# Kernel optimization log

Hardware: AMD Instinct MI355X
Metric: run time of the kernel (lower is better)

Reference implementation:

```python
import jax, jax.numpy as jnp
import numpy as np

H = 256        # hidden_channels
G = 13         # num_input_geofeature
E = 100000     # number of 2nd-order triplets
N = 50000      # num_nodes
DEPTH = 3      # finaldepth
EPS = 1e-5     # BatchNorm eps


def setup_inputs() -> dict:
    key = jax.random.key(0)
    ks = jax.random.split(key, 10)
    d_in = 3 * H + G  # 781
    return {
        "node_feature": jax.random.normal(ks[0], (N, H), jnp.float32),
        "geo_encoding": jax.random.normal(ks[1], (E, G), jnp.float32),
        "edge_index_2rd": jax.random.randint(ks[2], (3, E), 0, N),
        "edx_ij": jax.random.randint(ks[3], (E,), 0, 2 * E),
        "edx_jk": jax.random.randint(ks[4], (E,), 0, 2 * E),
        "att": jax.random.uniform(ks[5], (4,), jnp.float32),
        # 4 branches: layer0 (d_in->H) + DEPTH layers (H->H), xavier-ish init, zero bias
        "W0": jax.random.normal(ks[6], (4, d_in, H), jnp.float32) * (1.0 / np.sqrt(d_in)),
        "b0": jnp.zeros((4, H), jnp.float32),
        "Wh": jax.random.normal(ks[7], (4, DEPTH, H, H), jnp.float32) * (1.0 / np.sqrt(H)),
        "bh": jnp.zeros((4, DEPTH, H), jnp.float32),
        # BatchNorm (eval mode): affine params + running stats, one per layer per branch
        "gamma": jnp.ones((4, DEPTH + 1, H), jnp.float32),
        "beta": jnp.zeros((4, DEPTH + 1, H), jnp.float32),
        "run_mean": jnp.zeros((4, DEPTH + 1, H), jnp.float32),
        "run_var": jnp.ones((4, DEPTH + 1, H), jnp.float32),
        "num_edge_inside": E,
        "num_nodes": N,
    }


def _bn(h, g, b, m, v):
    return (h - m) * jax.lax.rsqrt(v + EPS) * g + b


def reference(node_feature, geo_encoding, edge_index_2rd, edx_ij, edx_jk, att,
              W0, b0, Wh, bh, gamma, beta, run_mean, run_var,
              num_edge_inside, num_nodes):
    i, j, k = edge_index_2rd[0], edge_index_2rd[1], edge_index_2rd[2]
    # gather node triplets + geo features -> [E, 3H+G]
    x = jnp.concatenate(
        [node_feature[i], node_feature[j], node_feature[k], geo_encoding], axis=-1)

    m_ij = edx_ij < num_edge_inside
    m_jk = edx_jk < num_edge_inside
    # 4 mutually-exclusive, exhaustive routing masks: [4, E]
    masks = jnp.stack([m_ij & m_jk, m_ij & ~m_jk, ~m_ij & m_jk, ~m_ij & ~m_jk])

    x_output = jnp.zeros((x.shape[0], H), x.dtype)
    for br in range(4):  # fixed small branch count
        h = jax.nn.relu(_bn(x @ W0[br] + b0[br],
                            gamma[br, 0], beta[br, 0], run_mean[br, 0], run_var[br, 0]))
        for l in range(DEPTH):
            h = jax.nn.relu(_bn(h @ Wh[br, l] + bh[br, l],
                                gamma[br, l + 1], beta[br, l + 1],
                                run_mean[br, l + 1], run_var[br, l + 1]))
        h = jax.nn.leaky_relu(h) * att[br]
        x_output = x_output + jnp.where(masks[br][:, None], h, jnp.zeros((), h.dtype))
    # scatter_add over target node index i -> [num_nodes, H]
    return jax.ops.segment_sum(x_output, i, num_segments=num_nodes)
```

## Files before the change

kernel.cpp:

```cpp
#include <hip/hip_runtime.h>
#include <hip/hip_bf16.h>
#include <stdint.h>

#define HCH 256
#define GEO 13
#define DEPTH 3
#define EPSBN 1e-5f
#define MFMA __builtin_amdgcn_mfma_f32_16x16x32_bf16

typedef __attribute__((ext_vector_type(8))) short short8;
typedef __attribute__((ext_vector_type(4))) float floatx4;

__device__ __forceinline__ short f2bs(float f) {
    unsigned u = __float_as_uint(f);
    unsigned r = (u + 0x7fffu + ((u >> 16) & 1u)) >> 16;
    return (short)r;
}

__global__ void k_zero(float4* out4, int n4, int* cnt) {
    int i = blockIdx.x * blockDim.x + threadIdx.x;
    if (i < n4) out4[i] = make_float4(0.f, 0.f, 0.f, 0.f);
    if (blockIdx.x == 0 && threadIdx.x < 4) cnt[threadIdx.x] = 0;
}

__global__ void k_prep(const float* __restrict__ W0, const float* __restrict__ Wh,
                       const float* __restrict__ b0, const float* __restrict__ bh,
                       const float* __restrict__ gm, const float* __restrict__ bt,
                       const float* __restrict__ mn, const float* __restrict__ vr,
                       const float* __restrict__ att,
                       const float* __restrict__ node, const float* __restrict__ geo,
                       const int* __restrict__ edx_ij, const int* __restrict__ edx_jk,
                       const int* __restrict__ nei_p,
                       short* __restrict__ W0t, short* __restrict__ Wht,
                       float* __restrict__ sc, float* __restrict__ of,
                       short* __restrict__ node_bf, short* __restrict__ geo_bf,
                       int* __restrict__ lists, int* __restrict__ cnt,
                       int E, int d_in_dim, int nb_node, int nb_geo) {
    const int B_W0 = 100, B_WH = 96, B_SC = 16;
    __shared__ short s[32][256];
    int b = blockIdx.x, t = threadIdx.x;
    if (b < B_W0) {
        int c = b % 25, br = b / 25;
        #pragma unroll
        for (int kk = 0; kk < 32; ++kk) {
            int kidx = c * 32 + kk;
            float v = (kidx < d_in_dim) ? W0[((size_t)br * d_in_dim + kidx) * HCH + t] : 0.f;
            s[kk][t] = f2bs(v);
        }
        __syncthreads();
        size_t obase = ((size_t)(b) * 256 + t) * 32;
        #pragma unroll
        for (int g = 0; g < 4; ++g) {
            short8 v;
            #pragma unroll
            for (int j = 0; j < 8; ++j) v[j] = s[g * 8 + j][t];
            *reinterpret_cast<short8*>(W0t + obase + g * 8) = v;
        }
    } else if (b < B_W0 + B_WH) {
        int idx = b - B_W0;
        int c = idx & 7; idx >>= 3;
        int l = idx % 3, br = idx / 3;
        #pragma unroll
        for (int kk = 0; kk < 32; ++kk) {
            float v = Wh[((size_t)(br * DEPTH + l) * HCH + (c * 32 + kk)) * HCH + t];
            s[kk][t] = f2bs(v);
        }
        __syncthreads();
        size_t obase = ((size_t)(b - B_W0) * 256 + t) * 32;
        #pragma unroll
        for (int g = 0; g < 4; ++g) {
            short8 v;
            #pragma unroll
            for (int j = 0; j < 8; ++j) v[j] = s[g * 8 + j][t];
            *reinterpret_cast<short8*>(Wht + obase + g * 8) = v;
        }
    } else if (b < B_W0 + B_WH + B_SC) {
        int idx = (b - B_W0 - B_WH) * 256 + t;
        int col = idx & 255, l = (idx >> 8) & 3, br = idx >> 10;
        int gi = (br * (DEPTH + 1) + l) * HCH + col;
        float sA = gm[gi] * rsqrtf(vr[gi] + EPSBN);
        float bias = (l == 0) ? b0[br * HCH + col] : bh[(br * DEPTH + (l - 1)) * HCH + col];
        float ofv = (bias - mn[gi]) * sA + bt[gi];
        if (l == 3) { float av = att[br]; sA *= av; ofv *= av; }
        sc[idx] = sA;
        of[idx] = ofv;
    } else if (b < B_W0 + B_WH + B_SC + nb_node) {
        size_t i = ((size_t)(b - B_W0 - B_WH - B_SC) * 256 + t) * 8;
        const float4* src = reinterpret_cast<const float4*>(node + i);
        float4 v0 = src[0], v1 = src[1];
        short8 pk;
        pk[0] = f2bs(v0.x); pk[1] = f2bs(v0.y); pk[2] = f2bs(v0.z); pk[3] = f2bs(v0.w);
        pk[4] = f2bs(v1.x); pk[5] = f2bs(v1.y); pk[6] = f2bs(v1.z); pk[7] = f2bs(v1.w);
        *reinterpret_cast<short8*>(node_bf + i) = pk;
    } else if (b < B_W0 + B_WH + B_SC + nb_node + nb_geo) {
        int i = (b - B_W0 - B_WH - B_SC - nb_node) * 256 + t;
        int e = i >> 2, cc = i & 3;
        if (e < E) {
            short8 pk;
            #pragma unroll
            for (int j = 0; j < 8; ++j) {
                int col = cc * 8 + j;
                pk[j] = (col < GEO) ? f2bs(geo[(size_t)e * GEO + col]) : (short)0;
            }
            *reinterpret_cast<short8*>(geo_bf + (size_t)e * 32 + cc * 8) = pk;
        }
    } else {
        int e = (b - (B_W0 + B_WH + B_SC + nb_node + nb_geo)) * 256 + t;
        int NEI = nei_p[0];
        int lane = t & 63;
        int br = -1;
        if (e < E)
            br = ((edx_ij[e] < NEI) ? 0 : 2) + ((edx_jk[e] < NEI) ? 0 : 1);
        unsigned long long lt = (lane == 63) ? 0x7fffffffffffffffull
                                             : ((1ull << lane) - 1ull);
        #pragma unroll
        for (int bb = 0; bb < 4; ++bb) {
            unsigned long long mk = __ballot(br == bb);
            if (mk) {
                int leader = __ffsll((long long)mk) - 1;
                int base = 0;
                if (lane == leader) base = atomicAdd(&cnt[bb], (int)__popcll(mk));
                base = __shfl(base, leader);
                if (br == bb) {
                    int pos = base + (int)__popcll(mk & lt);
                    lists[(size_t)bb * E + pos] = e;
                }
            }
        }
    }
}

__global__ __launch_bounds__(512)
void k_main(const short* __restrict__ node_bf, const short* __restrict__ geo_bf,
            const int* __restrict__ eidx,
            const short* __restrict__ W0t, const short* __restrict__ Wht,
            const float* __restrict__ sc, const float* __restrict__ of,
            const int* __restrict__ lists, const int* __restrict__ cnt,
            float* __restrict__ out, int E) {
    __shared__ __align__(16) short A[64][264];
    __shared__ int s_i[64];
    __shared__ int s_jk[2][64];
    __shared__ int s_e[64];

    int c0 = cnt[0], c1 = cnt[1], c2 = cnt[2], c3 = cnt[3];
    int t0 = (c0 + 63) >> 6, t1 = (c1 + 63) >> 6, t2 = (c2 + 63) >> 6, t3 = (c3 + 63) >> 6;
    int b = blockIdx.x;
    int br, tile, count;
    if (b < t0)                     { br = 0; tile = b;                count = c0; }
    else if (b < t0 + t1)           { br = 1; tile = b - t0;           count = c1; }
    else if (b < t0 + t1 + t2)      { br = 2; tile = b - t0 - t1;      count = c2; }
    else if (b < t0 + t1 + t2 + t3) { br = 3; tile = b - t0 - t1 - t2; count = c3; }
    else return;
    int m = count - tile * 64; if (m > 64) m = 64;

    int t = threadIdx.x;
    if (t < 64) {
        int e = (t < m) ? lists[(size_t)br * E + (size_t)tile * 64 + t] : 0;
        s_e[t] = (t < m) ? e : -1;
        s_i[t] = eidx[e];
        s_jk[0][t] = eidx[E + e];
        s_jk[1][t] = eidx[2 * E + e];
    }
    __syncthreads();

    int wv = t >> 6, lane = t & 63, quad = lane >> 4, l16 = lane & 15;
    int rbase = t >> 5, cc8 = (t & 31) * 8;

    floatx4 acc[4][2];
    #pragma unroll
    for (int rt = 0; rt < 4; ++rt)
        #pragma unroll
        for (int ct = 0; ct < 2; ++ct)
            #pragma unroll
            for (int r = 0; r < 4; ++r) acc[rt][ct][r] = 0.f;

    int boff[2];
    #pragma unroll
    for (int ct = 0; ct < 2; ++ct)
        boff[ct] = (wv * 32 + ct * 16 + l16) * 32 + quad * 8;

    auto do_chunks8 = [&](const short* Wbase) {
        short8 bb[3][2];
        #pragma unroll
        for (int ct = 0; ct < 2; ++ct) {
            bb[0][ct] = *reinterpret_cast<const short8*>(Wbase + boff[ct]);
            bb[1][ct] = *reinterpret_cast<const short8*>(Wbase + 8192 + boff[ct]);
        }
        #pragma unroll
        for (int c = 0; c < 8; ++c) {
            if (c + 2 < 8) {
                const short* Bn = Wbase + (size_t)(c + 2) * 8192;
                #pragma unroll
                for (int ct = 0; ct < 2; ++ct)
                    bb[(c + 2) % 3][ct] = *reinterpret_cast<const short8*>(Bn + boff[ct]);
            }
            short8 af[4];
            #pragma unroll
            for (int rt = 0; rt < 4; ++rt)
                af[rt] = *reinterpret_cast<const short8*>(&A[rt * 16 + l16][c * 32 + quad * 8]);
            #pragma unroll
            for (int rt = 0; rt < 4; ++rt)
                #pragma unroll
                for (int ct = 0; ct < 2; ++ct)
                    acc[rt][ct] = MFMA(af[rt], bb[c % 3][ct], acc[rt][ct], 0, 0, 0);
        }
    };
    auto do_chunk1 = [&](const short* Wbase) {
        short8 bc[2];
        #pragma unroll
        for (int ct = 0; ct < 2; ++ct)
            bc[ct] = *reinterpret_cast<const short8*>(Wbase + boff[ct]);
        short8 af[4];
        #pragma unroll
        for (int rt = 0; rt < 4; ++rt)
            af[rt] = *reinterpret_cast<const short8*>(&A[rt * 16 + l16][quad * 8]);
        #pragma unroll
        for (int rt = 0; rt < 4; ++rt)
            #pragma unroll
            for (int ct = 0; ct < 2; ++ct)
                acc[rt][ct] = MFMA(af[rt], bc[ct], acc[rt][ct], 0, 0, 0);
    };

    short8 g[2][4];
    short8 ggeo;
    {
        #pragma unroll
        for (int it = 0; it < 4; ++it)
            g[0][it] = *reinterpret_cast<const short8*>(
                node_bf + (size_t)s_i[it * 16 + rbase] * HCH + cc8);
    }
    int grow = t >> 2, gcc = t & 3;
    for (int p = 0; p < 4; ++p) {
        __syncthreads();
        if (p < 3) {
            #pragma unroll
            for (int it = 0; it < 4; ++it)
                *reinterpret_cast<short8*>(&A[it * 16 + rbase][cc8]) = g[p & 1][it];
        } else if (t < 256) {
            *reinterpret_cast<short8*>(&A[grow][gcc * 8]) = ggeo;
        }
        __syncthreads();
        if (p < 2) {
            const int* idxs = s_jk[p];
            #pragma unroll
            for (int it = 0; it < 4; ++it)
                g[(p + 1) & 1][it] = *reinterpret_cast<const short8*>(
                    node_bf + (size_t)idxs[it * 16 + rbase] * HCH + cc8);
        } else if (p == 2 && t < 256) {
            int e = s_e[grow];
            if (e >= 0)
                ggeo = *reinterpret_cast<const short8*>(geo_bf + (size_t)e * 32 + gcc * 8);
            else {
                #pragma unroll
                for (int j = 0; j < 8; ++j) ggeo[j] = 0;
            }
        }
        if (p < 3) do_chunks8(W0t + (size_t)(br * 25 + p * 8) * 8192);
        else       do_chunk1(W0t + (size_t)(br * 25 + 24) * 8192);
    }

    for (int l = 0; l < 4; ++l) {
        float sv[2], ov[2];
        #pragma unroll
        for (int ct = 0; ct < 2; ++ct) {
            int col = wv * 32 + ct * 16 + l16;
            sv[ct] = sc[(br * 4 + l) * HCH + col];
            ov[ct] = of[(br * 4 + l) * HCH + col];
        }
        if (l < 3) {
            __syncthreads();
            #pragma unroll
            for (int rt = 0; rt < 4; ++rt)
                #pragma unroll
                for (int ct = 0; ct < 2; ++ct) {
                    int col = wv * 32 + ct * 16 + l16;
                    #pragma unroll
                    for (int r = 0; r < 4; ++r) {
                        float h = fmaxf(acc[rt][ct][r] * sv[ct] + ov[ct], 0.f);
                        A[rt * 16 + quad * 4 + r][col] = f2bs(h);
                        acc[rt][ct][r] = 0.f;
                    }
                }
            __syncthreads();
            do_chunks8(Wht + (size_t)((br * 3 + l) * 8) * 8192);
        } else {
            #pragma unroll
            for (int rt = 0; rt < 4; ++rt)
                #pragma unroll
                for (int r = 0; r < 4; ++r) {
                    int row = rt * 16 + quad * 4 + r;
                    if (row < m) {
                        float* orow = out + (size_t)s_i[row] * HCH + wv * 32 + l16;
                        #pragma unroll
                        for (int ct = 0; ct < 2; ++ct) {
                            float h = fmaxf(acc[rt][ct][r] * sv[ct] + ov[ct], 0.f);
                            atomicAdd(orow + ct * 16, h);
                        }
                    }
                }
        }
    }
}

extern "C" void kernel_launch(void* const* d_in, const int* in_sizes, int n_in,
                              void* d_out, int out_size, void* d_ws, size_t ws_size,
                              hipStream_t stream) {
    const float* node  = (const float*)d_in[0];
    const float* geo   = (const float*)d_in[1];
    const int*   eidx  = (const int*)d_in[2];
    const int*   edxij = (const int*)d_in[3];
    const int*   edxjk = (const int*)d_in[4];
    const float* att   = (const float*)d_in[5];
    const float* W0    = (const float*)d_in[6];
    const float* b0    = (const float*)d_in[7];
    const float* Wh    = (const float*)d_in[8];
    const float* bh    = (const float*)d_in[9];
    const float* gm    = (const float*)d_in[10];
    const float* bt    = (const float*)d_in[11];
    const float* mn    = (const float*)d_in[12];
    const float* vr    = (const float*)d_in[13];
    const int*   neip  = (const int*)d_in[14];

    int E = in_sizes[3];
    int N = in_sizes[0] / HCH;
    int d_in_dim = in_sizes[6] / (4 * HCH);

    uint8_t* w = (uint8_t*)d_ws;
    size_t off = 0;
    short* W0t  = (short*)(w + off); off += (size_t)4 * 25 * 256 * 32 * 2;
    short* Wht  = (short*)(w + off); off += (size_t)4 * 3 * 8 * 256 * 32 * 2;
    float* sc   = (float*)(w + off); off += 4096 * 4;
    float* of   = (float*)(w + off); off += 4096 * 4;
    int*   lists= (int*)(w + off);   off += (size_t)4 * E * 4;
    int*   cnt  = (int*)(w + off);   off += 16;
    short* node_bf = (short*)(w + off); off += (size_t)N * HCH * 2;
    short* geo_bf  = (short*)(w + off); off += (size_t)E * 32 * 2;

    float* out = (float*)d_out;
    int n4 = out_size / 4;
    k_zero<<<(n4 + 255) / 256, 256, 0, stream>>>((float4*)out, n4, cnt);

    int nb_node = N / 8;
    int nb_geo  = (4 * E + 255) / 256;
    int nb_cmp  = (E + 255) / 256;
    k_prep<<<100 + 96 + 16 + nb_node + nb_geo + nb_cmp, 256, 0, stream>>>(
        W0, Wh, b0, bh, gm, bt, mn, vr, att, node, geo, edxij, edxjk, neip,
        W0t, Wht, sc, of, node_bf, geo_bf, lists, cnt, E, d_in_dim, nb_node, nb_geo);

    int T = (E >> 6) + 8;
    k_main<<<T, 512, 0, stream>>>(node_bf, geo_bf, eidx, W0t, Wht,
                                  sc, of, lists, cnt, out, E);
}
```

Measured before the change: 385.4 us.

## Double edge tile to 128 rows with XOR-swizzled LDS and direct global-to-LDS gathers

Each block now handles 128 edges instead of 64, with warps arranged 2x4 so each warp computes a 64x64 output sub-tile. Every weight fragment loaded from global memory now feeds twice as many MFMAs. Node rows are gathered straight into shared memory with global_load_lds, using an XOR swizzle to avoid bank conflicts, which replaces the register-staged gather. The register prefetch pipelining of weights and gathers is gone, and the larger accumulator array and LDS footprint may reduce occupancy.

Result: slower. 599.2 us (+55.5%).

```diff
diff --git a/kernel.cpp b/kernel.cpp
--- a/kernel.cpp
+++ b/kernel.cpp
@@ -10,6 +10,9 @@
 
 typedef __attribute__((ext_vector_type(8))) short short8;
 typedef __attribute__((ext_vector_type(4))) float floatx4;
+
+typedef __attribute__((address_space(1))) const void g_void;
+typedef __attribute__((address_space(3))) void l_void;
 
 __device__ __forceinline__ short f2bs(float f) {
     unsigned u = __float_as_uint(f);
@@ -130,20 +133,20 @@
     }
 }
 
-__global__ __launch_bounds__(512)
+__global__ __launch_bounds__(512, 4)
 void k_main(const short* __restrict__ node_bf, const short* __restrict__ geo_bf,
             const int* __restrict__ eidx,
             const short* __restrict__ W0t, const short* __restrict__ Wht,
             const float* __restrict__ sc, const float* __restrict__ of,
             const int* __restrict__ lists, const int* __restrict__ cnt,
             float* __restrict__ out, int E) {
-    __shared__ __align__(16) short A[64][264];
-    __shared__ int s_i[64];
-    __shared__ int s_jk[2][64];
-    __shared__ int s_e[64];
+    __shared__ __align__(16) short A[128][256];
+    __shared__ __align__(16) short Ageo[128][40];
+    __shared__ int s_idx[3][128];
+    __shared__ int s_e[128];
 
     int c0 = cnt[0], c1 = cnt[1], c2 = cnt[2], c3 = cnt[3];
-    int t0 = (c0 + 63) >> 6, t1 = (c1 + 63) >> 6, t2 = (c2 + 63) >> 6, t3 = (c3 + 63) >> 6;
+    int t0 = (c0 + 127) >> 7, t1 = (c1 + 127) >> 7, t2 = (c2 + 127) >> 7, t3 = (c3 + 127) >> 7;
     int b = blockIdx.x;
     int br, tile, count;
     if (b < t0)                     { br = 0; tile = b;                count = c0; }
@@ -151,133 +154,136 @@
     else if (b < t0 + t1 + t2)      { br = 2; tile = b - t0 - t1;      count = c2; }
     else if (b < t0 + t1 + t2 + t3) { br = 3; tile = b - t0 - t1 - t2; count = c3; }
     else return;
-    int m = count - tile * 64; if (m > 64) m = 64;
+    int m = count - tile * 128; if (m > 128) m = 128;
 
     int t = threadIdx.x;
-    if (t < 64) {
-        int e = (t < m) ? lists[(size_t)br * E + (size_t)tile * 64 + t] : 0;
+    if (t < 128) {
+        int e = (t < m) ? lists[(size_t)br * E + (size_t)tile * 128 + t] : 0;
         s_e[t] = (t < m) ? e : -1;
-        s_i[t] = eidx[e];
-        s_jk[0][t] = eidx[E + e];
-        s_jk[1][t] = eidx[2 * E + e];
+        s_idx[0][t] = eidx[e];
+        s_idx[1][t] = eidx[E + e];
+        s_idx[2][t] = eidx[2 * E + e];
     }
     __syncthreads();
 
-    int wv = t >> 6, lane = t & 63, quad = lane >> 4, l16 = lane & 15;
-    int rbase = t >> 5, cc8 = (t & 31) * 8;
-
-    floatx4 acc[4][2];
+    int wvid = t >> 6, lane = t & 63, quad = lane >> 4, l16 = lane & 15;
+    int wr = wvid >> 2, wc = wvid & 3;
+    int q16 = quad * 16;
+    int swz = (l16 & 7) << 4;
+
+    floatx4 acc[4][4];
     #pragma unroll
     for (int rt = 0; rt < 4; ++rt)
         #pragma unroll
-        for (int ct = 0; ct < 2; ++ct)
+        for (int ct = 0; ct < 4; ++ct)
             #pragma unroll
             for (int r = 0; r < 4; ++r) acc[rt][ct][r] = 0.f;
 
-    int boff[2];
+    int boff[4];
     #pragma unroll
-    for (int ct = 0; ct < 2; ++ct)
-        boff[ct] = (wv * 32 + ct * 16 + l16) * 32 + quad * 8;
+    for (int ct = 0; ct < 4; ++ct)
+        boff[ct] = (wc * 64 + ct * 16 + l16) * 32 + quad * 8;
+    int aoff[4];
+    #pragma unroll
+    for (int rt = 0; rt < 4; ++rt)
+        aoff[rt] = (wr * 64 + rt * 16 + l16) * 512;
+
+    const char* Ab = (const char*)&A[0][0];
+    char* Aw = (char*)&A[0][0];
+    short* Ag = &Ageo[0][0];
+
+    auto stage_nodes = [&](int p) {
+        const int* idxp = s_idx[p];
+        #pragma unroll
+        for (int i = 0; i < 8; ++i) {
+            int r0 = wvid * 16 + i * 2;
+            int row = r0 + (lane >> 5);
+            int e = idxp[row];
+            int soff = ((lane & 31) * 16) ^ ((row & 7) << 4);
+            const char* src = (const char*)(node_bf + (size_t)e * HCH) + soff;
+            __builtin_amdgcn_global_load_lds((g_void*)src, (l_void*)(&A[r0][0]), 16, 0, 0);
+        }
+    };
 
     auto do_chunks8 = [&](const short* Wbase) {
-        short8 bb[3][2];
-        #pragma unroll
-        for (int ct = 0; ct < 2; ++ct) {
-            bb[0][ct] = *reinterpret_cast<const short8*>(Wbase + boff[ct]);
-            bb[1][ct] = *reinterpret_cast<const short8*>(Wbase + 8192 + boff[ct]);
-        }
         #pragma unroll
         for (int c = 0; c < 8; ++c) {
-            if (c + 2 < 8) {
-                const short* Bn = Wbase + (size_t)(c + 2) * 8192;
+            short8 af[4];
+            #pragma unroll
+            for (int rt = 0; rt < 4; ++rt)
+                af[rt] = *reinterpret_cast<const short8*>(
+                    Ab + aoff[rt] + ((c * 64 + q16) ^ swz));
+            #pragma unroll
+            for (int ct = 0; ct < 4; ++ct) {
+                short8 bc = *reinterpret_cast<const short8*>(
+                    Wbase + (size_t)c * 8192 + boff[ct]);
                 #pragma unroll
-                for (int ct = 0; ct < 2; ++ct)
-                    bb[(c + 2) % 3][ct] = *reinterpret_cast<const short8*>(Bn + boff[ct]);
+                for (int rt = 0; rt < 4; ++rt)
+                    acc[rt][ct] = MFMA(af[rt], bc, acc[rt][ct], 0, 0, 0);
             }
-            short8 af[4];
+        }
+    };
+
+    {
+        int grow = t >> 2, gp = (t & 3) * 8;
+        int ge = s_e[grow];
+        short8 gv;
+        if (ge >= 0) gv = *reinterpret_cast<const short8*>(geo_bf + (size_t)ge * 32 + gp);
+        else {
+            #pragma unroll
+            for (int j = 0; j < 8; ++j) gv[j] = 0;
+        }
+        *reinterpret_cast<short8*>(Ag + grow * 40 + gp) = gv;
+    }
+    stage_nodes(0);
+    __syncthreads();
+
+    #pragma unroll
+    for (int p = 0; p < 3; ++p) {
+        do_chunks8(W0t + (size_t)(br * 25 + p * 8) * 8192);
+        if (p < 2) {
+            __syncthreads();
+            stage_nodes(p + 1);
+            __syncthreads();
+        }
+    }
+    {
+        short8 afg[4];
+        #pragma unroll
+        for (int rt = 0; rt < 4; ++rt)
+            afg[rt] = *reinterpret_cast<const short8*>(
+                Ag + (wr * 64 + rt * 16 + l16) * 40 + quad * 8);
+        const short* Wg = W0t + (size_t)(br * 25 + 24) * 8192;
+        #pragma unroll
+        for (int ct = 0; ct < 4; ++ct) {
+            short8 bc = *reinterpret_cast<const short8*>(Wg + boff[ct]);
             #pragma unroll
             for (int rt = 0; rt < 4; ++rt)
-                af[rt] = *reinterpret_cast<const short8*>(&A[rt * 16 + l16][c * 32 + quad * 8]);
+                acc[rt][ct] = MFMA(afg[rt], bc, acc[rt][ct], 0, 0, 0);
+        }
+    }
+
+    for (int l = 0; l < 4; ++l) {
+        float sv[4], ov[4];
+        #pragma unroll
+        for (int ct = 0; ct < 4; ++ct) {
+            int col = wc * 64 + ct * 16 + l16;
+            sv[ct] = sc[(br * 4 + l) * HCH + col];
+            ov[ct] = of[(br * 4 + l) * HCH + col];
+        }
+        if (l < 3) {
+            __syncthreads();
             #pragma unroll
             for (int rt = 0; rt < 4; ++rt)
                 #pragma unroll
-                for (int ct = 0; ct < 2; ++ct)
-                    acc[rt][ct] = MFMA(af[rt], bb[c % 3][ct], acc[rt][ct], 0, 0, 0);
-        }
-    };
-    auto do_chunk1 = [&](const short* Wbase) {
-        short8 bc[2];
-        #pragma unroll
-        for (int ct = 0; ct < 2; ++ct)
-            bc[ct] = *reinterpret_cast<const short8*>(Wbase + boff[ct]);
-        short8 af[4];
-        #pragma unroll
-        for (int rt = 0; rt < 4; ++rt)
-            af[rt] = *reinterpret_cast<const short8*>(&A[rt * 16 + l16][quad * 8]);
-        #pragma unroll
-        for (int rt = 0; rt < 4; ++rt)
-            #pragma unroll
-            for (int ct = 0; ct < 2; ++ct)
-                acc[rt][ct] = MFMA(af[rt], bc[ct], acc[rt][ct], 0, 0, 0);
-    };
-
-    short8 g[2][4];
-    short8 ggeo;
-    {
-        #pragma unroll
-        for (int it = 0; it < 4; ++it)
-            g[0][it] = *reinterpret_cast<const short8*>(
-                node_bf + (size_t)s_i[it * 16 + rbase] * HCH + cc8);
-    }
-    int grow = t >> 2, gcc = t & 3;
-    for (int p = 0; p < 4; ++p) {
-        __syncthreads();
-        if (p < 3) {
-            #pragma unroll
-            for (int it = 0; it < 4; ++it)
-                *reinterpret_cast<short8*>(&A[it * 16 + rbase][cc8]) = g[p & 1][it];
-        } else if (t < 256) {
-            *reinterpret_cast<short8*>(&A[grow][gcc * 8]) = ggeo;
-        }
-        __syncthreads();
-        if (p < 2) {
-            const int* idxs = s_jk[p];
-            #pragma unroll
-            for (int it = 0; it < 4; ++it)
-                g[(p + 1) & 1][it] = *reinterpret_cast<const short8*>(
-                    node_bf + (size_t)idxs[it * 16 + rbase] * HCH + cc8);
-        } else if (p == 2 && t < 256) {
-            int e = s_e[grow];
-            if (e >= 0)
-                ggeo = *reinterpret_cast<const short8*>(geo_bf + (size_t)e * 32 + gcc * 8);
-            else {
-                #pragma unroll
-                for (int j = 0; j < 8; ++j) ggeo[j] = 0;
-            }
-        }
-        if (p < 3) do_chunks8(W0t + (size_t)(br * 25 + p * 8) * 8192);
-        else       do_chunk1(W0t + (size_t)(br * 25 + 24) * 8192);
-    }
-
-    for (int l = 0; l < 4; ++l) {
-        float sv[2], ov[2];
-        #pragma unroll
-        for (int ct = 0; ct < 2; ++ct) {
-            int col = wv * 32 + ct * 16 + l16;
-            sv[ct] = sc[(br * 4 + l) * HCH + col];
-            ov[ct] = of[(br * 4 + l) * HCH + col];
-        }
-        if (l < 3) {
-            __syncthreads();
-            #pragma unroll
-            for (int rt = 0; rt < 4; ++rt)
-                #pragma unroll
-                for (int ct = 0; ct < 2; ++ct) {
-                    int col = wv * 32 + ct * 16 + l16;
+                for (int ct = 0; ct < 4; ++ct) {
+                    int colb = (wc * 64 + ct * 16 + l16) * 2;
                     #pragma unroll
                     for (int r = 0; r < 4; ++r) {
+                        int row = wr * 64 + rt * 16 + quad * 4 + r;
                         float h = fmaxf(acc[rt][ct][r] * sv[ct] + ov[ct], 0.f);
-                        A[rt * 16 + quad * 4 + r][col] = f2bs(h);
+                        *reinterpret_cast<short*>(
+                            Aw + row * 512 + (colb ^ ((row & 7) << 4))) = f2bs(h);
                         acc[rt][ct][r] = 0.f;
                     }
                 }
@@ -288,11 +294,11 @@
             for (int rt = 0; rt < 4; ++rt)
                 #pragma unroll
                 for (int r = 0; r < 4; ++r) {
-                    int row = rt * 16 + quad * 4 + r;
+                    int row = wr * 64 + rt * 16 + quad * 4 + r;
                     if (row < m) {
-                        float* orow = out + (size_t)s_i[row] * HCH + wv * 32 + l16;
+                        float* orow = out + (size_t)s_idx[0][row] * HCH + wc * 64 + l16;
                         #pragma unroll
-                        for (int ct = 0; ct < 2; ++ct) {
+                        for (int ct = 0; ct < 4; ++ct) {
                             float h = fmaxf(acc[rt][ct][r] * sv[ct] + ov[ct], 0.f);
                             atomicAdd(orow + ct * 16, h);
                         }
@@ -347,7 +353,7 @@
         W0, Wh, b0, bh, gm, bt, mn, vr, att, node, geo, edxij, edxjk, neip,
         W0t, Wht, sc, of, node_bf, geo_bf, lists, cnt, E, d_in_dim, nb_node, nb_geo);
 
-    int T = (E >> 6) + 8;
+    int T = (E >> 7) + 8;
     k_main<<<T, 512, 0, stream>>>(node_bf, geo_bf, eidx, W0t, Wht,
                                   sc, of, lists, cnt, out, E);
 }
```

## Swizzle LDS tile, separate geo buffer, deepen weight prefetch, fold zeroing into prep

Applied to the files above, without the earlier changes.

Replaces the padded LDS activation tile with an XOR-swizzled unpadded layout to avoid bank conflicts, and moves the geo features into a separate small LDS buffer that is loaded up front. The weight register prefetch ring grows from 3 to 4 stages, and MFMA bursts are wrapped in s_setprio. The output-zeroing kernel is merged into the prep kernel, with a memset for the counters. This saves one launch and some LDS stalls, at the cost of more registers and extra address arithmetic.

New measurement: 409.4 us. +6.2%, slower.

```diff
diff --git a/kernel.cpp b/kernel.cpp
--- a/kernel.cpp
+++ b/kernel.cpp
@@ -15,12 +15,6 @@
     unsigned u = __float_as_uint(f);
     unsigned r = (u + 0x7fffu + ((u >> 16) & 1u)) >> 16;
     return (short)r;
-}
-
-__global__ void k_zero(float4* out4, int n4, int* cnt) {
-    int i = blockIdx.x * blockDim.x + threadIdx.x;
-    if (i < n4) out4[i] = make_float4(0.f, 0.f, 0.f, 0.f);
-    if (blockIdx.x == 0 && threadIdx.x < 4) cnt[threadIdx.x] = 0;
 }
 
 __global__ void k_prep(const float* __restrict__ W0, const float* __restrict__ Wh,
@@ -35,7 +29,8 @@
                        float* __restrict__ sc, float* __restrict__ of,
                        short* __restrict__ node_bf, short* __restrict__ geo_bf,
                        int* __restrict__ lists, int* __restrict__ cnt,
-                       int E, int d_in_dim, int nb_node, int nb_geo) {
+                       float4* __restrict__ outz, int n4out,
+                       int E, int d_in_dim, int nb_node, int nb_geo, int nb_out) {
     const int B_W0 = 100, B_WH = 96, B_SC = 16;
     __shared__ short s[32][256];
     int b = blockIdx.x, t = threadIdx.x;
@@ -104,8 +99,11 @@
             }
             *reinterpret_cast<short8*>(geo_bf + (size_t)e * 32 + cc * 8) = pk;
         }
+    } else if (b < B_W0 + B_WH + B_SC + nb_node + nb_geo + nb_out) {
+        int i = (b - (B_W0 + B_WH + B_SC + nb_node + nb_geo)) * 256 + t;
+        if (i < n4out) outz[i] = make_float4(0.f, 0.f, 0.f, 0.f);
     } else {
-        int e = (b - (B_W0 + B_WH + B_SC + nb_node + nb_geo)) * 256 + t;
+        int e = (b - (B_W0 + B_WH + B_SC + nb_node + nb_geo + nb_out)) * 256 + t;
         int NEI = nei_p[0];
         int lane = t & 63;
         int br = -1;
@@ -137,9 +135,9 @@
             const float* __restrict__ sc, const float* __restrict__ of,
             const int* __restrict__ lists, const int* __restrict__ cnt,
             float* __restrict__ out, int E) {
-    __shared__ __align__(16) short A[64][264];
-    __shared__ int s_i[64];
-    __shared__ int s_jk[2][64];
+    __shared__ __align__(16) short A[64][256];
+    __shared__ __align__(16) short Ageo[64][40];
+    __shared__ int s_idx[3][64];
     __shared__ int s_e[64];
 
     int c0 = cnt[0], c1 = cnt[1], c2 = cnt[2], c3 = cnt[3];
@@ -157,14 +155,15 @@
     if (t < 64) {
         int e = (t < m) ? lists[(size_t)br * E + (size_t)tile * 64 + t] : 0;
         s_e[t] = (t < m) ? e : -1;
-        s_i[t] = eidx[e];
-        s_jk[0][t] = eidx[E + e];
-        s_jk[1][t] = eidx[2 * E + e];
+        s_idx[0][t] = eidx[e];
+        s_idx[1][t] = eidx[E + e];
+        s_idx[2][t] = eidx[2 * E + e];
     }
     __syncthreads();
 
     int wv = t >> 6, lane = t & 63, quad = lane >> 4, l16 = lane & 15;
     int rbase = t >> 5, cc8 = (t & 31) * 8;
+    int swz = (l16 & 7) << 4;
 
     floatx4 acc[4][2];
     #pragma unroll
@@ -179,30 +178,38 @@
     for (int ct = 0; ct < 2; ++ct)
         boff[ct] = (wv * 32 + ct * 16 + l16) * 32 + quad * 8;
 
+    const char* Ab = (const char*)&A[0][0];
+    char* Aw = (char*)&A[0][0];
+    short* Ag = &Ageo[0][0];
+
     auto do_chunks8 = [&](const short* Wbase) {
-        short8 bb[3][2];
-        #pragma unroll
-        for (int ct = 0; ct < 2; ++ct) {
-            bb[0][ct] = *reinterpret_cast<const short8*>(Wbase + boff[ct]);
-            bb[1][ct] = *reinterpret_cast<const short8*>(Wbase + 8192 + boff[ct]);
-        }
+        short8 bb[4][2];
+        #pragma unroll
+        for (int s = 0; s < 3; ++s)
+            #pragma unroll
+            for (int ct = 0; ct < 2; ++ct)
+                bb[s][ct] = *reinterpret_cast<const short8*>(
+                    Wbase + (size_t)s * 8192 + boff[ct]);
         #pragma unroll
         for (int c = 0; c < 8; ++c) {
-            if (c + 2 < 8) {
-                const short* Bn = Wbase + (size_t)(c + 2) * 8192;
+            if (c + 3 < 8) {
+                const short* Bn = Wbase + (size_t)(c + 3) * 8192;
                 #pragma unroll
                 for (int ct = 0; ct < 2; ++ct)
-                    bb[(c + 2) % 3][ct] = *reinterpret_cast<const short8*>(Bn + boff[ct]);
+                    bb[(c + 3) & 3][ct] = *reinterpret_cast<const short8*>(Bn + boff[ct]);
             }
             short8 af[4];
             #pragma unroll
             for (int rt = 0; rt < 4; ++rt)
-                af[rt] = *reinterpret_cast<const short8*>(&A[rt * 16 + l16][c * 32 + quad * 8]);
+                af[rt] = *reinterpret_cast<const short8*>(
+                    Ab + (rt * 16 + l16) * 512 + ((c * 64 + quad * 16) ^ swz));
+            __builtin_amdgcn_s_setprio(1);
             #pragma unroll
             for (int rt = 0; rt < 4; ++rt)
                 #pragma unroll
                 for (int ct = 0; ct < 2; ++ct)
-                    acc[rt][ct] = MFMA(af[rt], bb[c % 3][ct], acc[rt][ct], 0, 0, 0);
+                    acc[rt][ct] = MFMA(af[rt], bb[c & 3][ct], acc[rt][ct], 0, 0, 0);
+            __builtin_amdgcn_s_setprio(0);
         }
     };
     auto do_chunk1 = [&](const short* Wbase) {
@@ -213,51 +220,54 @@
         short8 af[4];
         #pragma unroll
         for (int rt = 0; rt < 4; ++rt)
-            af[rt] = *reinterpret_cast<const short8*>(&A[rt * 16 + l16][quad * 8]);
+            af[rt] = *reinterpret_cast<const short8*>(
+                Ag + (rt * 16 + l16) * 40 + quad * 8);
+        __builtin_amdgcn_s_setprio(1);
         #pragma unroll
         for (int rt = 0; rt < 4; ++rt)
             #pragma unroll
             for (int ct = 0; ct < 2; ++ct)
                 acc[rt][ct] = MFMA(af[rt], bc[ct], acc[rt][ct], 0, 0, 0);
+        __builtin_amdgcn_s_setprio(0);
     };
 
+    if (t < 256) {
+        int grow = t >> 2, gp = (t & 3) * 8;
+        int ge = s_e[grow];
+        short8 gv;
+        if (ge >= 0) gv = *reinterpret_cast<const short8*>(geo_bf + (size_t)ge * 32 + gp);
+        else {
+            #pragma unroll
+            for (int j = 0; j < 8; ++j) gv[j] = 0;
+        }
+        *reinterpret_cast<short8*>(Ag + grow * 40 + gp) = gv;
+    }
     short8 g[2][4];
-    short8 ggeo;
-    {
-        #pragma unroll
-        for (int it = 0; it < 4; ++it)
-            g[0][it] = *reinterpret_cast<const short8*>(
-                node_bf + (size_t)s_i[it * 16 + rbase] * HCH + cc8);
-    }
-    int grow = t >> 2, gcc = t & 3;
-    for (int p = 0; p < 4; ++p) {
+    #pragma unroll
+    for (int it = 0; it < 4; ++it)
+        g[0][it] = *reinterpret_cast<const short8*>(
+            node_bf + (size_t)s_idx[0][it * 16 + rbase] * HCH + cc8);
+
+    #pragma unroll
+    for (int p = 0; p < 3; ++p) {
         __syncthreads();
-        if (p < 3) {
-            #pragma unroll
-            for (int it = 0; it < 4; ++it)
-                *reinterpret_cast<short8*>(&A[it * 16 + rbase][cc8]) = g[p & 1][it];
-        } else if (t < 256) {
-            *reinterpret_cast<short8*>(&A[grow][gcc * 8]) = ggeo;
+        #pragma unroll
+        for (int it = 0; it < 4; ++it) {
+            int row = it * 16 + rbase;
+            *reinterpret_cast<short8*>(
+                Aw + row * 512 + ((cc8 * 2) ^ ((row & 7) << 4))) = g[p & 1][it];
         }
         __syncthreads();
         if (p < 2) {
-            const int* idxs = s_jk[p];
+            const int* idxs = s_idx[p + 1];
             #pragma unroll
             for (int it = 0; it < 4; ++it)
                 g[(p + 1) & 1][it] = *reinterpret_cast<const short8*>(
                     node_bf + (size_t)idxs[it * 16 + rbase] * HCH + cc8);
-        } else if (p == 2 && t < 256) {
-            int e = s_e[grow];
-            if (e >= 0)
-                ggeo = *reinterpret_cast<const short8*>(geo_bf + (size_t)e * 32 + gcc * 8);
-            else {
-                #pragma unroll
-                for (int j = 0; j < 8; ++j) ggeo[j] = 0;
-            }
-        }
-        if (p < 3) do_chunks8(W0t + (size_t)(br * 25 + p * 8) * 8192);
-        else       do_chunk1(W0t + (size_t)(br * 25 + 24) * 8192);
-    }
+        }
+        do_chunks8(W0t + (size_t)(br * 25 + p * 8) * 8192);
+    }
+    do_chunk1(W0t + (size_t)(br * 25 + 24) * 8192);
 
     for (int l = 0; l < 4; ++l) {
         float sv[2], ov[2];
@@ -273,11 +283,13 @@
             for (int rt = 0; rt < 4; ++rt)
                 #pragma unroll
                 for (int ct = 0; ct < 2; ++ct) {
-                    int col = wv * 32 + ct * 16 + l16;
+                    int colb = (wv * 32 + ct * 16 + l16) * 2;
                     #pragma unroll
                     for (int r = 0; r < 4; ++r) {
+                        int row = rt * 16 + quad * 4 + r;
                         float h = fmaxf(acc[rt][ct][r] * sv[ct] + ov[ct], 0.f);
-                        A[rt * 16 + quad * 4 + r][col] = f2bs(h);
+                        *reinterpret_cast<short*>(
+                            Aw + row * 512 + (colb ^ ((row & 7) << 4))) = f2bs(h);
                         acc[rt][ct][r] = 0.f;
                     }
                 }
@@ -290,7 +302,7 @@
                 for (int r = 0; r < 4; ++r) {
                     int row = rt * 16 + quad * 4 + r;
                     if (row < m) {
-                        float* orow = out + (size_t)s_i[row] * HCH + wv * 32 + l16;
+                        float* orow = out + (size_t)s_idx[0][row] * HCH + wv * 32 + l16;
                         #pragma unroll
                         for (int ct = 0; ct < 2; ++ct) {
                             float h = fmaxf(acc[rt][ct][r] * sv[ct] + ov[ct], 0.f);
@@ -338,14 +350,17 @@
 
     float* out = (float*)d_out;
     int n4 = out_size / 4;
-    k_zero<<<(n4 + 255) / 256, 256, 0, stream>>>((float4*)out, n4, cnt);
+
+    hipMemsetAsync(cnt, 0, 16, stream);
 
     int nb_node = N / 8;
     int nb_geo  = (4 * E + 255) / 256;
+    int nb_out  = (n4 + 255) / 256;
     int nb_cmp  = (E + 255) / 256;
-    k_prep<<<100 + 96 + 16 + nb_node + nb_geo + nb_cmp, 256, 0, stream>>>(
+    k_prep<<<100 + 96 + 16 + nb_node + nb_geo + nb_out + nb_cmp, 256, 0, stream>>>(
         W0, Wh, b0, bh, gm, bt, mn, vr, att, node, geo, edxij, edxjk, neip,
-        W0t, Wht, sc, of, node_bf, geo_bf, lists, cnt, E, d_in_dim, nb_node, nb_geo);
+        W0t, Wht, sc, of, node_bf, geo_bf, lists, cnt,
+        (float4*)out, n4, E, d_in_dim, nb_node, nb_geo, nb_out);
 
     int T = (E >> 6) + 8;
     k_main<<<T, 512, 0, stream>>>(node_bf, geo_bf, eidx, W0t, Wht,
```
